# Optimization experiments

Measured on AMD Instinct MI355X. Metric: run time of the kernel, lower is better.

The kernel has to match this reference:

```python
import jax, jax.numpy as jnp
import numpy as np

B, N, D = 4, 4096, 1024
H, S, R = 16, 256, 2           # heads, segment size, dilation rate
DH = D // H
LN_EPS = 1e-5


def _hilbert_perm(n_side):
    # perm[d] = linear index (y*side + x) of the d-th point on the Hilbert curve
    def d2xy(n, d):
        x = y = 0
        t = d
        s = 1
        while s < n:
            rx = 1 & (t // 2)
            ry = 1 & (t ^ rx)
            if ry == 0:
                if rx == 1:
                    x = s - 1 - x
                    y = s - 1 - y
                x, y = y, x
            x += s * rx
            y += s * ry
            t //= 4
            s *= 2
        return x, y
    perm = np.empty(n_side * n_side, dtype=np.int32)
    for d in range(n_side * n_side):
        xx, yy = d2xy(n_side, d)
        perm[d] = yy * n_side + xx
    return perm


def setup_inputs() -> dict:
    key = jax.random.key(0)
    ks = jax.random.split(key, 8)
    sc = 0.02
    return {
        "x": jax.random.normal(ks[0], (B, N, D), jnp.float32),
        "ln1_g": jnp.ones((D,), jnp.float32),
        "ln1_b": jnp.zeros((D,), jnp.float32),
        "w_qkv": jax.random.normal(ks[1], (D, 3 * D), jnp.float32) * sc,
        "b_qkv": jnp.zeros((3 * D,), jnp.float32),
        "w_o": jax.random.normal(ks[2], (D, D), jnp.float32) * sc,
        "b_o": jnp.zeros((D,), jnp.float32),
        "ln2_g": jnp.ones((D,), jnp.float32),
        "ln2_b": jnp.zeros((D,), jnp.float32),
        "w1": jax.random.normal(ks[3], (D, 4 * D), jnp.float32) * sc,
        "b1": jnp.zeros((4 * D,), jnp.float32),
        "w2": jax.random.normal(ks[4], (4 * D, D), jnp.float32) * sc,
        "b2": jnp.zeros((D,), jnp.float32),
        "hilbert_perm": jnp.asarray(_hilbert_perm(int(np.sqrt(N)))),
    }


def _layernorm(x, g, b):
    mu = jnp.mean(x, axis=-1, keepdims=True)
    var = jnp.mean(jnp.square(x - mu), axis=-1, keepdims=True)
    return (x - mu) * jax.lax.rsqrt(var + LN_EPS) * g + b


def _hilbert_dilated_attention(x, w_qkv, b_qkv, w_o, b_o, perm):
    b, n, d = x.shape
    nseg, sr = n // S, S // R
    xp = jnp.take(x, perm, axis=1)                    # Hilbert reorder
    qkv = xp @ w_qkv + b_qkv                          # [b,n,3d]
    q, k, v = jnp.split(qkv, 3, axis=-1)
    def seg(t):
        return t.reshape(b, nseg, S, H, DH)
    q, k, v = seg(q), seg(k), seg(v)
    # per-head dilation offset: head h attends positions (h % R) :: R in each segment
    offs = jnp.arange(H, dtype=jnp.int32) % R                        # [H]
    idx = offs[None, :] + R * jnp.arange(sr, dtype=jnp.int32)[:, None]  # [sr,H]
    idx_g = idx[None, None, :, :, None]                              # [1,1,sr,H,1]
    qd = jnp.take_along_axis(q, idx_g, axis=2)        # [b,nseg,sr,H,dh]
    kd = jnp.take_along_axis(k, idx_g, axis=2)
    vd = jnp.take_along_axis(v, idx_g, axis=2)
    scores = jnp.einsum('bgqhd,bgkhd->bghqk', qd, kd) / jnp.sqrt(jnp.asarray(DH, x.dtype))
    attn = jax.nn.softmax(scores, axis=-1)
    od = jnp.einsum('bghqk,bgkhd->bgqhd', attn, vd)   # [b,nseg,sr,H,dh]
    # scatter back into full segments; uncovered (head,pos) slots stay zero
    out = jnp.zeros((b, nseg, S, H, DH), x.dtype)
    out = out.at[:, :, idx, jnp.arange(H)[None, :], :].set(od)
    out = out.reshape(b, n, d) @ w_o + b_o
    inv = jnp.argsort(perm)
    return jnp.take(out, inv, axis=1)                 # inverse Hilbert reorder


def reference(x, ln1_g, ln1_b, w_qkv, b_qkv, w_o, b_o, ln2_g, ln2_b, w1, b1, w2, b2, hilbert_perm):
    h = _layernorm(x, ln1_g, ln1_b)
    h = _hilbert_dilated_attention(h, w_qkv, b_qkv, w_o, b_o, hilbert_perm)
    x = x + h
    h = _layernorm(x, ln2_g, ln2_b)
    h = jax.nn.gelu(h @ w1 + b1, approximate=False) @ w2 + b2
    return x + h
```

## Files before the change

### kernel.cpp

```cpp
#include <hip/hip_runtime.h>

typedef short bf16x8 __attribute__((ext_vector_type(8)));
typedef float f32x4 __attribute__((ext_vector_type(4)));
typedef unsigned short u16;

#define GLDS16(g, l) __builtin_amdgcn_global_load_lds( \
    (const __attribute__((address_space(1))) void*)(g), \
    (__attribute__((address_space(3))) void*)(l), 16, 0, 0)

__device__ __forceinline__ u16 f2b(float f) {
  unsigned u = __float_as_uint(f);
  u += 0x7fffu + ((u >> 16) & 1u);
  return (u16)(u >> 16);
}

__global__ __launch_bounds__(256)
void transpose_bf16(const float* __restrict__ w, u16* __restrict__ wt, int K, int N) {
  __shared__ float tile[32][33];
  const int n0 = blockIdx.x * 32, k0 = blockIdx.y * 32;
  const int tx = threadIdx.x & 31, ty = threadIdx.x >> 5;
#pragma unroll
  for (int i = 0; i < 4; ++i)
    tile[ty + i * 8][tx] = w[(size_t)(k0 + ty + i * 8) * N + n0 + tx];
  __syncthreads();
#pragma unroll
  for (int i = 0; i < 4; ++i)
    wt[(size_t)(n0 + ty + i * 8) * K + k0 + tx] = f2b(tile[tx][ty + i * 8]);
}

__global__ __launch_bounds__(256)
void ln_rows(const float* __restrict__ src, const float* __restrict__ gam,
             const float* __restrict__ bet, const int* __restrict__ perm,
             u16* __restrict__ dst) {
  const int orow = blockIdx.x;
  const int b = orow >> 12, j = orow & 4095;
  const int srow = perm ? ((b << 12) + perm[j]) : orow;
  const float4 v = ((const float4*)(src + (size_t)srow * 1024))[threadIdx.x];
  float s = v.x + v.y + v.z + v.w;
  float s2 = v.x * v.x + v.y * v.y + v.z * v.z + v.w * v.w;
#pragma unroll
  for (int d = 1; d < 64; d <<= 1) { s += __shfl_xor(s, d); s2 += __shfl_xor(s2, d); }
  __shared__ float rs[4], rs2[4];
  const int wave = threadIdx.x >> 6, lane = threadIdx.x & 63;
  if (lane == 0) { rs[wave] = s; rs2[wave] = s2; }
  __syncthreads();
  s = rs[0] + rs[1] + rs[2] + rs[3];
  s2 = rs2[0] + rs2[1] + rs2[2] + rs2[3];
  const float mu = s * (1.f / 1024.f);
  const float var = s2 * (1.f / 1024.f) - mu * mu;
  const float rstd = rsqrtf(var + 1e-5f);
  const int c = threadIdx.x * 4;
  const float4 gg = *(const float4*)(gam + c);
  const float4 bb = *(const float4*)(bet + c);
  const u16 o0 = f2b((v.x - mu) * rstd * gg.x + bb.x);
  const u16 o1 = f2b((v.y - mu) * rstd * gg.y + bb.y);
  const u16 o2 = f2b((v.z - mu) * rstd * gg.z + bb.z);
  const u16 o3 = f2b((v.w - mu) * rstd * gg.w + bb.w);
  const unsigned lo = (unsigned)o0 | ((unsigned)o1 << 16);
  const unsigned hi = (unsigned)o2 | ((unsigned)o3 << 16);
  *(uint2*)(dst + (size_t)orow * 1024 + c) = make_uint2(lo, hi);
}

template <int EPI>
__global__ __launch_bounds__(512, 2)
void gemm256(const u16* __restrict__ A, const u16* __restrict__ Bt,
             const float* __restrict__ bias, void* __restrict__ Cout,
             const float* __restrict__ resid, const int* __restrict__ perm,
             int M, int Nn, int K) {
  __shared__ u16 sm[65536];
  char* const smc = (char*)sm;
  const int tid = threadIdx.x;
  const int w = tid >> 6, lane = tid & 63;
  const int lr = lane & 15, lg = lane >> 4;
  const int wm = w >> 2, wn = w & 3;

  int wg = blockIdx.x;
  const int nwg = gridDim.x;
  if ((nwg & 7) == 0) { const int per = nwg >> 3; wg = (wg & 7) * per + (wg >> 3); }
  const int gx = M >> 8;
  const int m0 = (wg % gx) << 8, n0 = (wg / gx) << 8;

  const int srow = tid >> 3;
  const int scol = ((tid & 7) ^ (srow & 7)) << 3;
  const size_t aSrc = (size_t)(m0 + srow) * K + scol;
  const size_t bSrc = (size_t)(n0 + srow) * K + scol;
  char* const lWav = smc + w * 1024;

  const int slot0 = (lg ^ (lr & 7)) << 4;
  const int aRow = (wm * 128 + lr) * 128;
  const int bRow = (wn * 64 + lr) * 128 + 32768;

  const int NT = K >> 6;

#define STAGE_(d, mat, h, k0) do { \
    const u16* gp = ((mat) ? Bt : A) + ((mat) ? bSrc : aSrc) + (size_t)(h) * 128 * K + (k0); \
    char* lp = lWav + (d) * 65536 + (mat) * 32768 + (h) * 16384; \
    GLDS16(gp, lp); GLDS16(gp + (size_t)64 * K, lp + 8192); } while (0)

#define BAR_() do { asm volatile("" ::: "memory"); __builtin_amdgcn_s_barrier(); \
                    asm volatile("" ::: "memory"); } while (0)

  STAGE_(0, 1, 0, 0); STAGE_(0, 1, 1, 0); STAGE_(0, 0, 0, 0); STAGE_(0, 0, 1, 0);
  if (NT > 1) {
    STAGE_(1, 1, 0, 64); STAGE_(1, 1, 1, 64); STAGE_(1, 0, 0, 64);
    asm volatile("s_waitcnt vmcnt(6)" ::: "memory");
  } else {
    asm volatile("s_waitcnt vmcnt(0)" ::: "memory");
  }
  BAR_();

  f32x4 acc[8][4] = {};
  bf16x8 a[8], b[8];

  for (int t = 0; t < NT; ++t) {
    const int c = t & 1;
    const char* pA = smc + c * 65536 + aRow;
    const char* pB = smc + c * 65536 + bRow;

#pragma unroll
    for (int mf = 0; mf < 4; ++mf)
#pragma unroll
      for (int kk = 0; kk < 2; ++kk)
        a[mf * 2 + kk] = *(const bf16x8*)(pA + mf * 2048 + (slot0 ^ (kk << 6)));
#pragma unroll
    for (int nf = 0; nf < 4; ++nf)
#pragma unroll
      for (int kk = 0; kk < 2; ++kk)
        b[nf * 2 + kk] = *(const bf16x8*)(pB + nf * 2048 + (slot0 ^ (kk << 6)));
    if (t + 1 < NT) STAGE_(c ^ 1, 0, 1, (t + 1) << 6);
    BAR_();
    __builtin_amdgcn_s_setprio(1);
#pragma unroll
    for (int mf = 0; mf < 4; ++mf)
#pragma unroll
      for (int nf = 0; nf < 2; ++nf)
#pragma unroll
        for (int kk = 0; kk < 2; ++kk)
          acc[mf][nf] = __builtin_amdgcn_mfma_f32_16x16x32_bf16(a[mf * 2 + kk], b[nf * 2 + kk], acc[mf][nf], 0, 0, 0);
    __builtin_amdgcn_s_setprio(0);
    BAR_();

    if (t + 2 < NT) STAGE_(c, 1, 0, (t + 2) << 6);
    BAR_();
    __builtin_amdgcn_s_setprio(1);
#pragma unroll
    for (int mf = 0; mf < 4; ++mf)
#pragma unroll
      for (int nf = 0; nf < 2; ++nf)
#pragma unroll
        for (int kk = 0; kk < 2; ++kk)
          acc[mf][2 + nf] = __builtin_amdgcn_mfma_f32_16x16x32_bf16(a[mf * 2 + kk], b[(2 + nf) * 2 + kk], acc[mf][2 + nf], 0, 0, 0);
    __builtin_amdgcn_s_setprio(0);
    BAR_();

#pragma unroll
    for (int mf = 0; mf < 4; ++mf)
#pragma unroll
      for (int kk = 0; kk < 2; ++kk)
        a[mf * 2 + kk] = *(const bf16x8*)(pA + (4 + mf) * 2048 + (slot0 ^ (kk << 6)));
    if (t + 2 < NT) STAGE_(c, 1, 1, (t + 2) << 6);
    BAR_();
    __builtin_amdgcn_s_setprio(1);
#pragma unroll
    for (int mf = 0; mf < 4; ++mf)
#pragma unroll
      for (int nf = 0; nf < 2; ++nf)
#pragma unroll
        for (int kk = 0; kk < 2; ++kk)
          acc[4 + mf][nf] = __builtin_amdgcn_mfma_f32_16x16x32_bf16(a[mf * 2 + kk], b[nf * 2 + kk], acc[4 + mf][nf], 0, 0, 0);
    __builtin_amdgcn_s_setprio(0);
    BAR_();

    if (t + 2 < NT) STAGE_(c, 0, 0, (t + 2) << 6);
    if (t < NT - 2) asm volatile("s_waitcnt vmcnt(6)" ::: "memory");
    else            asm volatile("s_waitcnt vmcnt(0)" ::: "memory");
    BAR_();
    __builtin_amdgcn_s_setprio(1);
#pragma unroll
    for (int mf = 0; mf < 4; ++mf)
#pragma unroll
      for (int nf = 0; nf < 2; ++nf)
#pragma unroll
        for (int kk = 0; kk < 2; ++kk)
          acc[4 + mf][2 + nf] = __builtin_amdgcn_mfma_f32_16x16x32_bf16(a[mf * 2 + kk], b[(2 + nf) * 2 + kk], acc[4 + mf][2 + nf], 0, 0, 0);
    __builtin_amdgcn_s_setprio(0);
    BAR_();
  }
#undef STAGE_
#undef BAR_

#pragma unroll
  for (int mf = 0; mf < 8; ++mf) {
#pragma unroll
    for (int nf = 0; nf < 4; ++nf) {
      const int col = n0 + wn * 64 + nf * 16 + lr;
      const float bia = bias[col];
#pragma unroll
      for (int r = 0; r < 4; ++r) {
        const int row = m0 + wm * 128 + mf * 16 + lg * 4 + r;
        float v = acc[mf][nf][r] + bia;
        if (EPI == 0) {
          ((u16*)Cout)[(size_t)row * Nn + col] = f2b(v);
        } else if (EPI == 1) {
          v = 0.5f * v * (1.f + erff(v * 0.70710678118654752f));
          ((u16*)Cout)[(size_t)row * Nn + col] = f2b(v);
        } else if (EPI == 2) {
          const int b = row >> 12, j = row & 4095;
          const size_t di = ((size_t)((b << 12) + perm[j])) * 1024 + col;
          ((float*)Cout)[di] = resid[di] + v;
        } else {
          const size_t di = (size_t)row * 1024 + col;
          ((float*)Cout)[di] = resid[di] + v;
        }
      }
    }
  }
}

__global__ __launch_bounds__(256, 2)
void attn_kernel(const u16* __restrict__ qkv, u16* __restrict__ outp) {
  const int blk = blockIdx.x;
  const int h = blk & 15, g = (blk >> 4) & 15, b = blk >> 8;
  const int tid = threadIdx.x, wave = tid >> 6, lane = tid & 63;
  const int lr = lane & 15, lg = lane >> 4;
  const int par = h & 1;

  __shared__ u16 lQ[128 * 64];
  __shared__ u16 lK[128 * 64];
  __shared__ u16 lVt[64 * 128];
  __shared__ u16 lP[4][32 * 128];

  const size_t rbase = (size_t)((b << 12) + (g << 8) + par);

#pragma unroll
  for (int i = 0; i < 4; ++i) {
    const int ou = i * 4096 + wave * 1024;
    const int o = ou + lane * 16;
    const int j = o >> 7, cb = o & 127;
    const u16* gq = qkv + (rbase + 2 * j) * 3072 + h * 64 + (cb >> 1);
    GLDS16(gq, (char*)lQ + ou);
    GLDS16(gq + 1024, (char*)lK + ou);
  }
#pragma unroll
  for (int i = 0; i < 4; ++i) {
    const int c = tid + i * 256;
    const int j = c >> 3, dc = c & 7;
    const uint4 vv = *(const uint4*)(qkv + (rbase + 2 * j) * 3072 + 2048 + h * 64 + dc * 8);
    const u16* pv = (const u16*)&vv;
#pragma unroll
    for (int e = 0; e < 8; ++e) lVt[(dc * 8 + e) * 128 + j] = pv[e];
  }
  __syncthreads();

  f32x4 sacc[2][8] = {};
#pragma unroll
  for (int kk = 0; kk < 2; ++kk) {
    bf16x8 aq[2], bk[8];
#pragma unroll
    for (int mf = 0; mf < 2; ++mf)
      aq[mf] = *(const bf16x8*)&lQ[(wave * 32 + mf * 16 + lr) * 64 + kk * 32 + lg * 8];
#pragma unroll
    for (int nf = 0; nf < 8; ++nf)
      bk[nf] = *(const bf16x8*)&lK[(nf * 16 + lr) * 64 + kk * 32 + lg * 8];
#pragma unroll
    for (int mf = 0; mf < 2; ++mf)
#pragma unroll
      for (int nf = 0; nf < 8; ++nf)
        sacc[mf][nf] = __builtin_amdgcn_mfma_f32_16x16x32_bf16(aq[mf], bk[nf], sacc[mf][nf], 0, 0, 0);
  }

#pragma unroll
  for (int mf = 0; mf < 2; ++mf) {
#pragma unroll
    for (int r = 0; r < 4; ++r) {
      float mx = -3e38f;
#pragma unroll
      for (int nf = 0; nf < 8; ++nf) mx = fmaxf(mx, sacc[mf][nf][r]);
#pragma unroll
      for (int d = 1; d < 16; d <<= 1) mx = fmaxf(mx, __shfl_xor(mx, d));
      float pv[8];
      float sum = 0.f;
#pragma unroll
      for (int nf = 0; nf < 8; ++nf) {
        pv[nf] = __expf((sacc[mf][nf][r] - mx) * 0.125f);
        sum += pv[nf];
      }
#pragma unroll
      for (int d = 1; d < 16; d <<= 1) sum += __shfl_xor(sum, d);
      const float inv = 1.f / sum;
      const int rrow = mf * 16 + lg * 4 + r;
#pragma unroll
      for (int nf = 0; nf < 8; ++nf)
        lP[wave][rrow * 128 + nf * 16 + lr] = f2b(pv[nf] * inv);
    }
  }
  __syncthreads();

  f32x4 oacc[2][4] = {};
#pragma unroll
  for (int kk = 0; kk < 4; ++kk) {
    bf16x8 ap[2], bv[4];
#pragma unroll
    for (int mf = 0; mf < 2; ++mf)
      ap[mf] = *(const bf16x8*)&lP[wave][(mf * 16 + lr) * 128 + kk * 32 + lg * 8];
#pragma unroll
    for (int nf = 0; nf < 4; ++nf)
      bv[nf] = *(const bf16x8*)&lVt[(nf * 16 + lr) * 128 + kk * 32 + lg * 8];
#pragma unroll
    for (int mf = 0; mf < 2; ++mf)
#pragma unroll
      for (int nf = 0; nf < 4; ++nf)
        oacc[mf][nf] = __builtin_amdgcn_mfma_f32_16x16x32_bf16(ap[mf], bv[nf], oacc[mf][nf], 0, 0, 0);
  }

  u16* obase = outp + ((size_t)((b << 12) + (g << 8))) * 1024 + h * 64;
#pragma unroll
  for (int mf = 0; mf < 2; ++mf)
#pragma unroll
    for (int nf = 0; nf < 4; ++nf)
#pragma unroll
      for (int r = 0; r < 4; ++r) {
        const int jq = wave * 32 + mf * 16 + lg * 4 + r;
        obase[(size_t)(par + 2 * jq) * 1024 + nf * 16 + lr] = f2b(oacc[mf][nf][r]);
      }
  const int jz = tid >> 1, hh = (tid & 1) * 32;
  u16* zp = obase + (size_t)((1 - par) + 2 * jz) * 1024 + hh;
  const uint4 z = make_uint4(0u, 0u, 0u, 0u);
#pragma unroll
  for (int i = 0; i < 4; ++i) ((uint4*)zp)[i] = z;
}

extern "C" void kernel_launch(void* const* d_in, const int* in_sizes, int n_in,
                              void* d_out, int out_size, void* d_ws, size_t ws_size,
                              hipStream_t stream) {
  const float* x    = (const float*)d_in[0];
  const float* ln1g = (const float*)d_in[1];
  const float* ln1b = (const float*)d_in[2];
  const float* wqkv = (const float*)d_in[3];
  const float* bqkv = (const float*)d_in[4];
  const float* wo   = (const float*)d_in[5];
  const float* bo   = (const float*)d_in[6];
  const float* ln2g = (const float*)d_in[7];
  const float* ln2b = (const float*)d_in[8];
  const float* w1   = (const float*)d_in[9];
  const float* b1   = (const float*)d_in[10];
  const float* w2   = (const float*)d_in[11];
  const float* b2   = (const float*)d_in[12];
  const int*   perm = (const int*)d_in[13];
  float* out = (float*)d_out;
  char* ws = (char*)d_ws;

  u16*  r0    = (u16*)ws;
  u16*  qkv   = (u16*)(ws + (32ull << 20));
  u16*  a1    = (u16*)(ws + (32ull << 20));
  float* x2   = (float*)(ws + (160ull << 20));
  u16*  wqkvT = (u16*)(ws + (224ull << 20));
  u16*  woT   = (u16*)(ws + (230ull << 20));
  u16*  w1T   = (u16*)(ws + (232ull << 20));
  u16*  w2T   = (u16*)(ws + (240ull << 20));

  transpose_bf16<<<dim3(3072 / 32, 1024 / 32), 256, 0, stream>>>(wqkv, wqkvT, 1024, 3072);
  transpose_bf16<<<dim3(1024 / 32, 1024 / 32), 256, 0, stream>>>(wo, woT, 1024, 1024);
  transpose_bf16<<<dim3(4096 / 32, 1024 / 32), 256, 0, stream>>>(w1, w1T, 1024, 4096);
  transpose_bf16<<<dim3(1024 / 32, 4096 / 32), 256, 0, stream>>>(w2, w2T, 4096, 1024);

  ln_rows<<<16384, 256, 0, stream>>>(x, ln1g, ln1b, perm, r0);
  gemm256<0><<<(16384 / 256) * (3072 / 256), 512, 0, stream>>>(r0, wqkvT, bqkv, qkv, nullptr, nullptr,
                                                               16384, 3072, 1024);
  attn_kernel<<<1024, 256, 0, stream>>>(qkv, r0);
  gemm256<2><<<(16384 / 256) * (1024 / 256), 512, 0, stream>>>(r0, woT, bo, x2, x, perm,
                                                               16384, 1024, 1024);
  ln_rows<<<16384, 256, 0, stream>>>(x2, ln2g, ln2b, nullptr, r0);
  gemm256<1><<<(16384 / 256) * (4096 / 256), 512, 0, stream>>>(r0, w1T, b1, a1, nullptr, nullptr,
                                                               16384, 4096, 1024);
  gemm256<3><<<(16384 / 256) * (1024 / 256), 512, 0, stream>>>(a1, w2T, b2, out, x2, nullptr,
                                                               16384, 1024, 4096);
}
```

Measured before the change: 612.0 us.

## Spread LDS fragment reads across MFMA phases and prefetch next tile's fragments

```diff
diff --git a/kernel.cpp b/kernel.cpp
--- a/kernel.cpp
+++ b/kernel.cpp
@@ -100,6 +100,27 @@
 #define BAR_() do { asm volatile("" ::: "memory"); __builtin_amdgcn_s_barrier(); \
                     asm volatile("" ::: "memory"); } while (0)
 
+  bf16x8 aLo[8], aHi[8], bb[8];
+
+#define R_ALO(P) do { _Pragma("unroll") for (int mf = 0; mf < 4; ++mf) \
+    _Pragma("unroll") for (int kk = 0; kk < 2; ++kk) \
+      aLo[mf * 2 + kk] = *(const bf16x8*)((P) + mf * 2048 + (slot0 ^ (kk << 6))); } while (0)
+#define R_AHI(P) do { _Pragma("unroll") for (int mf = 0; mf < 4; ++mf) \
+    _Pragma("unroll") for (int kk = 0; kk < 2; ++kk) \
+      aHi[mf * 2 + kk] = *(const bf16x8*)((P) + (4 + mf) * 2048 + (slot0 ^ (kk << 6))); } while (0)
+#define R_B01(P) do { _Pragma("unroll") for (int nf = 0; nf < 2; ++nf) \
+    _Pragma("unroll") for (int kk = 0; kk < 2; ++kk) \
+      bb[nf * 2 + kk] = *(const bf16x8*)((P) + nf * 2048 + (slot0 ^ (kk << 6))); } while (0)
+#define R_B23(P) do { _Pragma("unroll") for (int nf = 0; nf < 2; ++nf) \
+    _Pragma("unroll") for (int kk = 0; kk < 2; ++kk) \
+      bb[4 + nf * 2 + kk] = *(const bf16x8*)((P) + (2 + nf) * 2048 + (slot0 ^ (kk << 6))); } while (0)
+
+#define C_QUAD(AARR, NB, MB) do { _Pragma("unroll") for (int mf = 0; mf < 4; ++mf) \
+    _Pragma("unroll") for (int nf = 0; nf < 2; ++nf) \
+    _Pragma("unroll") for (int kk = 0; kk < 2; ++kk) \
+      acc[(MB) * 4 + mf][(NB) * 2 + nf] = __builtin_amdgcn_mfma_f32_16x16x32_bf16( \
+          AARR[mf * 2 + kk], bb[(NB) * 4 + nf * 2 + kk], acc[(MB) * 4 + mf][(NB) * 2 + nf], 0, 0, 0); } while (0)
+
   STAGE_(0, 1, 0, 0); STAGE_(0, 1, 1, 0); STAGE_(0, 0, 0, 0); STAGE_(0, 0, 1, 0);
   if (NT > 1) {
     STAGE_(1, 1, 0, 64); STAGE_(1, 1, 1, 64); STAGE_(1, 0, 0, 64);
@@ -110,64 +131,36 @@
   BAR_();
 
   f32x4 acc[8][4] = {};
-  bf16x8 a[8], b[8];
+  R_ALO(smc + aRow);
+  R_B01(smc + bRow);
 
   for (int t = 0; t < NT; ++t) {
     const int c = t & 1;
-    const char* pA = smc + c * 65536 + aRow;
-    const char* pB = smc + c * 65536 + bRow;
-
-#pragma unroll
-    for (int mf = 0; mf < 4; ++mf)
-#pragma unroll
-      for (int kk = 0; kk < 2; ++kk)
-        a[mf * 2 + kk] = *(const bf16x8*)(pA + mf * 2048 + (slot0 ^ (kk << 6)));
-#pragma unroll
-    for (int nf = 0; nf < 4; ++nf)
-#pragma unroll
-      for (int kk = 0; kk < 2; ++kk)
-        b[nf * 2 + kk] = *(const bf16x8*)(pB + nf * 2048 + (slot0 ^ (kk << 6)));
+    const char* cA = smc + c * 65536 + aRow;
+    const char* cB = smc + c * 65536 + bRow;
+    const char* nA = smc + (c ^ 1) * 65536 + aRow;
+    const char* nB = smc + (c ^ 1) * 65536 + bRow;
+
+    R_B23(cB);
     if (t + 1 < NT) STAGE_(c ^ 1, 0, 1, (t + 1) << 6);
     BAR_();
     __builtin_amdgcn_s_setprio(1);
-#pragma unroll
-    for (int mf = 0; mf < 4; ++mf)
-#pragma unroll
-      for (int nf = 0; nf < 2; ++nf)
-#pragma unroll
-        for (int kk = 0; kk < 2; ++kk)
-          acc[mf][nf] = __builtin_amdgcn_mfma_f32_16x16x32_bf16(a[mf * 2 + kk], b[nf * 2 + kk], acc[mf][nf], 0, 0, 0);
+    C_QUAD(aLo, 0, 0);
     __builtin_amdgcn_s_setprio(0);
     BAR_();
 
+    R_AHI(cA);
     if (t + 2 < NT) STAGE_(c, 1, 0, (t + 2) << 6);
     BAR_();
     __builtin_amdgcn_s_setprio(1);
-#pragma unroll
-    for (int mf = 0; mf < 4; ++mf)
-#pragma unroll
-      for (int nf = 0; nf < 2; ++nf)
-#pragma unroll
-        for (int kk = 0; kk < 2; ++kk)
-          acc[mf][2 + nf] = __builtin_amdgcn_mfma_f32_16x16x32_bf16(a[mf * 2 + kk], b[(2 + nf) * 2 + kk], acc[mf][2 + nf], 0, 0, 0);
+    C_QUAD(aLo, 1, 0);
     __builtin_amdgcn_s_setprio(0);
     BAR_();
 
-#pragma unroll
-    for (int mf = 0; mf < 4; ++mf)
-#pragma unroll
-      for (int kk = 0; kk < 2; ++kk)
-        a[mf * 2 + kk] = *(const bf16x8*)(pA + (4 + mf) * 2048 + (slot0 ^ (kk << 6)));
     if (t + 2 < NT) STAGE_(c, 1, 1, (t + 2) << 6);
     BAR_();
     __builtin_amdgcn_s_setprio(1);
-#pragma unroll
-    for (int mf = 0; mf < 4; ++mf)
-#pragma unroll
-      for (int nf = 0; nf < 2; ++nf)
-#pragma unroll
-        for (int kk = 0; kk < 2; ++kk)
-          acc[4 + mf][nf] = __builtin_amdgcn_mfma_f32_16x16x32_bf16(a[mf * 2 + kk], b[nf * 2 + kk], acc[4 + mf][nf], 0, 0, 0);
+    C_QUAD(aHi, 0, 1);
     __builtin_amdgcn_s_setprio(0);
     BAR_();
 
@@ -175,19 +168,19 @@
     if (t < NT - 2) asm volatile("s_waitcnt vmcnt(6)" ::: "memory");
     else            asm volatile("s_waitcnt vmcnt(0)" ::: "memory");
     BAR_();
+    if (t + 1 < NT) { R_ALO(nA); R_B01(nB); }
     __builtin_amdgcn_s_setprio(1);
-#pragma unroll
-    for (int mf = 0; mf < 4; ++mf)
-#pragma unroll
-      for (int nf = 0; nf < 2; ++nf)
-#pragma unroll
-        for (int kk = 0; kk < 2; ++kk)
-          acc[4 + mf][2 + nf] = __builtin_amdgcn_mfma_f32_16x16x32_bf16(a[mf * 2 + kk], b[(2 + nf) * 2 + kk], acc[4 + mf][2 + nf], 0, 0, 0);
+    C_QUAD(aHi, 1, 1);
     __builtin_amdgcn_s_setprio(0);
     BAR_();
   }
 #undef STAGE_
 #undef BAR_
+#undef R_ALO
+#undef R_AHI
+#undef R_B01
+#undef R_B23
+#undef C_QUAD
 
 #pragma unroll
   for (int mf = 0; mf < 8; ++mf) {
```

After: 612.1 us. About the same (+0.0%).
